# Performance work log

Measured on AMD Instinct MI355X. Metric: run time of the kernel, lower is better.

## Reference

```python
import jax, jax.numpy as jnp
import numpy as np

N_NODES = 100000
N_EDGES = 600000
N_ETYPES = 3
N_LAYERS = 3  # n_layers + 1 conv layers
D = 128
EPS = 1e-5


def setup_inputs() -> dict:
    key = jax.random.key(0)
    ks = jax.random.split(key, 8)
    scale = 1.0 / np.sqrt(D)
    x = jax.random.normal(ks[0], (N_NODES, D), dtype=jnp.float32)
    src = jax.random.randint(ks[1], (N_ETYPES, N_EDGES), 0, N_NODES, dtype=jnp.int32)
    dst = jax.random.randint(ks[2], (N_ETYPES, N_EDGES), 0, N_NODES, dtype=jnp.int32)
    W_self = jax.random.normal(ks[3], (N_LAYERS, N_ETYPES, D, D), dtype=jnp.float32) * scale
    W_neigh = jax.random.normal(ks[4], (N_LAYERS, N_ETYPES, D, D), dtype=jnp.float32) * scale
    b = jax.random.normal(ks[5], (N_LAYERS, N_ETYPES, D), dtype=jnp.float32) * 0.01
    gamma = jnp.ones((N_LAYERS, D), dtype=jnp.float32)
    beta = jnp.zeros((N_LAYERS, D), dtype=jnp.float32)
    return {"x": x, "src": src, "dst": dst, "W_self": W_self, "W_neigh": W_neigh,
            "b": b, "gamma": gamma, "beta": beta}


def reference(x, src, dst, W_self, W_neigh, b, gamma, beta):
    N = x.shape[0]
    L, K = W_self.shape[0], W_self.shape[1]
    # in-degree per etype (DGL mean aggregator: zero-degree -> 0 neighbor feat)
    degs = [jnp.clip(jax.ops.segment_sum(jnp.ones((dst.shape[1],), x.dtype), dst[k],
                                         num_segments=N), 1.0, None)
            for k in range(K)]
    h = x
    for l in range(L):
        acc = jnp.zeros((N, W_self.shape[-1]), x.dtype)
        for k in range(K):
            # gather src feats, mean-aggregate onto dst: [N, D]
            neigh = jax.ops.segment_sum(h[src[k]], dst[k], num_segments=N) / degs[k][:, None]
            o = h @ W_self[l, k] + neigh @ W_neigh[l, k] + b[l, k]
            if l < L - 1:  # activation inside SAGEConv, last layer has none
                o = jax.nn.relu(o)
            acc = acc + o  # HeteroGraphConv aggregate='sum'
        # BatchNorm1d, training mode (biased batch variance)
        mu = acc.mean(axis=0)
        var = ((acc - mu) ** 2).mean(axis=0)
        h = gamma[l] * (acc - mu) / jnp.sqrt(var + EPS) + beta[l]
    return h
```

## Files before the change

kernel.cpp:

```cpp
#include <hip/hip_runtime.h>

#define NN 100000
#define NNP 100096
#define NE 600000
#define KE 3
#define NL 3
#define D  128
#define EPS 1e-5f
#define NB 391
#define NBKT 196
#define EPB 4096
#define NEB 147
#define NSL 16

typedef __attribute__((ext_vector_type(8))) short short8;
typedef __attribute__((ext_vector_type(4))) float floatx4;

__device__ __forceinline__ void atomic_add_f32(float* p, float v) { unsafeAtomicAdd(p, v); }

__device__ __forceinline__ float bf2f(unsigned int u16) {
    unsigned int v = u16 << 16;
    return __builtin_bit_cast(float, v);
}
__device__ __forceinline__ unsigned int f2bf(float f) {
    unsigned int u = __builtin_bit_cast(unsigned int, f);
    u += 0x7FFFu + ((u >> 16) & 1u);
    return u >> 16;
}
__device__ __forceinline__ unsigned int pack2(float a, float b) {
    return f2bf(a) | (f2bf(b) << 16);
}

__global__ void convert_x_kernel(const float* __restrict__ x, ushort* __restrict__ hbf) {
    size_t i = (size_t)blockIdx.x * blockDim.x + threadIdx.x;
    if (i >= (size_t)NN * D / 4) return;
    float4 v = *(const float4*)(x + i * 4);
    uint2 o;
    o.x = pack2(v.x, v.y);
    o.y = pack2(v.z, v.w);
    *(uint2*)(hbf + i * 4) = o;
}

__global__ void wprep_kernel(const float* __restrict__ Ws, const float* __restrict__ Wn,
                             ushort* __restrict__ Bt) {
    int idx = blockIdx.x * blockDim.x + threadIdx.x;
    if (idx >= NL * KE * 128 * 256) return;
    int lk  = idx >> 15;
    int rem = idx & 32767;
    int n   = rem >> 8;
    int kk  = rem & 255;
    float v = (kk < 128) ? Ws[(size_t)lk * 16384 + kk * 128 + n]
                         : Wn[(size_t)lk * 16384 + (kk - 128) * 128 + n];
    Bt[idx] = (ushort)f2bf(v);
}

__global__ void bucket_count_kernel(const int* __restrict__ dst,
                                    int* __restrict__ bucketTotal, int* __restrict__ blockBase) {
    const int blk = blockIdx.x;
    const int k = blk / NEB, cb = blk - k * NEB;
    __shared__ int hist[NBKT];
    for (int i = threadIdx.x; i < NBKT; i += 256) hist[i] = 0;
    __syncthreads();
    const int e0 = cb * EPB, e1 = min(e0 + EPB, NE);
    for (int e = e0 + threadIdx.x; e < e1; e += 256)
        atomicAdd(&hist[dst[(size_t)k * NE + e] >> 9], 1);
    __syncthreads();
    for (int i = threadIdx.x; i < NBKT; i += 256) {
        int c = hist[i];
        int base = c ? atomicAdd(&bucketTotal[k * NBKT + i], c) : 0;
        blockBase[(size_t)blk * NBKT + i] = base;
    }
}

__global__ void bucket_scan_kernel(const int* __restrict__ bucketTotal,
                                   int* __restrict__ bucketStart) {
    __shared__ int sd[1024];
    const int t = threadIdx.x;
    int v = (t < KE * NBKT) ? bucketTotal[t] : 0;
    sd[t] = v;
    __syncthreads();
    for (int off = 1; off < 1024; off <<= 1) {
        int u = (t >= off) ? sd[t - off] : 0;
        __syncthreads();
        sd[t] += u;
        __syncthreads();
    }
    if (t < KE * NBKT) bucketStart[t] = sd[t] - v;
}

__global__ void bucket_scatter_kernel(const int* __restrict__ src, const int* __restrict__ dst,
                                      const int* __restrict__ bucketStart,
                                      const int* __restrict__ blockBase,
                                      uint2* __restrict__ ebuf) {
    const int blk = blockIdx.x;
    const int k = blk / NEB, cb = blk - k * NEB;
    __shared__ int hist[NBKT], binoff[NBKT], cur[NBKT];
    __shared__ int sc[256];
    __shared__ uint2 stage[EPB];
    const int t = threadIdx.x;
    for (int i = t; i < NBKT; i += 256) hist[i] = 0;
    __syncthreads();
    const int e0 = cb * EPB, e1 = min(e0 + EPB, NE);
    for (int e = e0 + t; e < e1; e += 256)
        atomicAdd(&hist[dst[(size_t)k * NE + e] >> 9], 1);
    __syncthreads();
    int hv = (t < NBKT) ? hist[t] : 0;
    sc[t] = hv;
    __syncthreads();
    for (int off = 1; off < 256; off <<= 1) {
        int u = (t >= off) ? sc[t - off] : 0;
        __syncthreads();
        sc[t] += u;
        __syncthreads();
    }
    if (t < NBKT) { binoff[t] = sc[t] - hv; cur[t] = sc[t] - hv; }
    __syncthreads();
    for (int e = e0 + t; e < e1; e += 256) {
        int d = dst[(size_t)k * NE + e], s = src[(size_t)k * NE + e];
        int b = d >> 9;
        int p = atomicAdd(&cur[b], 1);
        stage[p] = make_uint2((unsigned)s, (unsigned)d);
    }
    __syncthreads();
    const int n = e1 - e0;
    for (int i = t; i < n; i += 256) {
        uint2 ed = stage[i];
        int b = (int)(ed.y >> 9);
        int pos = bucketStart[k * NBKT + b] + blockBase[(size_t)blk * NBKT + b] + (i - binoff[b]);
        ebuf[pos] = ed;
    }
}

__global__ void bucket_deg_kernel(const uint2* __restrict__ ebuf,
                                  const int* __restrict__ bucketStart, int* __restrict__ degi) {
    const int blk = blockIdx.x;
    const int k = blk / NBKT, b = blk - k * NBKT;
    __shared__ int cnt[512];
    for (int i = threadIdx.x; i < 512; i += 256) cnt[i] = 0;
    __syncthreads();
    const int s0 = bucketStart[blk];
    const int s1 = (blk + 1 < KE * NBKT) ? bucketStart[blk + 1] : KE * NE;
    for (int e = s0 + threadIdx.x; e < s1; e += 256)
        atomicAdd(&cnt[ebuf[e].y & 511], 1);
    __syncthreads();
    const int n0 = b << 9;
    for (int i = threadIdx.x; i < 512; i += 256) {
        int node = n0 + i;
        if (node < NN) degi[(size_t)k * NN + node] = cnt[i];
    }
}

__global__ void scan_a_kernel(const int* __restrict__ degi, int* __restrict__ bsum) {
    const int b = blockIdx.x;
    const int k = b / NB, lb = b - k * NB;
    const int t = threadIdx.x;
    const int i = lb * 256 + t;
    int deg = (i < NN) ? degi[(size_t)k * NN + i] : 0;
    __shared__ int sd[256];
    sd[t] = deg;
    __syncthreads();
    for (int off = 128; off > 0; off >>= 1) {
        if (t < off) sd[t] += sd[t + off];
        __syncthreads();
    }
    if (t == 0) bsum[b] = sd[0];
}

__global__ void scan_b_kernel(int* __restrict__ bsum) {
    const int k = blockIdx.x;
    const int t = threadIdx.x;
    int v = (t < NB) ? bsum[k * NB + t] : 0;
    __shared__ int sd[512];
    sd[t] = v;
    __syncthreads();
    for (int off = 1; off < 512; off <<= 1) {
        int u = (t >= off) ? sd[t - off] : 0;
        __syncthreads();
        sd[t] += u;
        __syncthreads();
    }
    if (t < NB) bsum[k * NB + t] = sd[t] - v;
}

__global__ void scan_c_kernel(const int* __restrict__ degi, const int* __restrict__ bsum,
                              int* __restrict__ rowptr, float* __restrict__ invdeg) {
    const int b = blockIdx.x;
    const int k = b / NB, lb = b - k * NB;
    const int t = threadIdx.x;
    const int i = lb * 256 + t;
    int deg = (i < NN) ? degi[(size_t)k * NN + i] : 0;
    __shared__ int sd[256];
    sd[t] = deg;
    __syncthreads();
    for (int off = 1; off < 256; off <<= 1) {
        int u = (t >= off) ? sd[t - off] : 0;
        __syncthreads();
        sd[t] += u;
        __syncthreads();
    }
    int val = bsum[b] + sd[t] - deg;
    if (i < NN) {
        rowptr[(size_t)k * (NN + 1) + i] = val;
        invdeg[(size_t)k * NN + i] = 1.0f / (float)max(deg, 1);
    }
    if (i == NN) rowptr[(size_t)k * (NN + 1) + NN] = NE;
}

__global__ void bucket_fill_kernel(const uint2* __restrict__ ebuf,
                                   const int* __restrict__ bucketStart,
                                   const int* __restrict__ rowptr, int* __restrict__ csr) {
    const int blk = blockIdx.x;
    const int k = blk / NBKT, b = blk - k * NBKT;
    __shared__ int cur[512];
    const int n0 = b << 9;
    for (int i = threadIdx.x; i < 512; i += 256) {
        int node = n0 + i;
        cur[i] = (node < NN) ? rowptr[(size_t)k * (NN + 1) + node] : 0;
    }
    __syncthreads();
    const int s0 = bucketStart[blk];
    const int s1 = (blk + 1 < KE * NBKT) ? bucketStart[blk + 1] : KE * NE;
    for (int e = s0 + threadIdx.x; e < s1; e += 256) {
        uint2 ed = ebuf[e];
        int p = atomicAdd(&cur[ed.y & 511], 1);
        csr[(size_t)k * NE + p] = (int)ed.x;
    }
}

__global__ void gather3_kernel(const ushort* __restrict__ hbf, const int* __restrict__ csr,
                               const int* __restrict__ rowptr, const float* __restrict__ invdeg,
                               ushort* __restrict__ neigh) {
    int g = blockIdx.x * 16 + (threadIdx.x >> 4);
    if (g >= KE * NN) return;
    int k = g / NN, node = g - k * NN;
    const int q = (threadIdx.x & 15) * 8;
    const int* rp = rowptr + (size_t)k * (NN + 1) + node;
    const int* cs = csr + (size_t)k * NE;
    int beg = rp[0], end = rp[1];
    float f0=0,f1=0,f2=0,f3=0,f4=0,f5=0,f6=0,f7=0;
    int j = beg;
    for (; j + 4 <= end; j += 4) {
        int s0 = cs[j], s1 = cs[j + 1], s2 = cs[j + 2], s3 = cs[j + 3];
        uint4 a = *(const uint4*)(hbf + (size_t)s0 * D + q);
        uint4 b = *(const uint4*)(hbf + (size_t)s1 * D + q);
        uint4 c = *(const uint4*)(hbf + (size_t)s2 * D + q);
        uint4 d = *(const uint4*)(hbf + (size_t)s3 * D + q);
        f0 += bf2f(a.x & 0xffff) + bf2f(b.x & 0xffff) + bf2f(c.x & 0xffff) + bf2f(d.x & 0xffff);
        f1 += bf2f(a.x >> 16)    + bf2f(b.x >> 16)    + bf2f(c.x >> 16)    + bf2f(d.x >> 16);
        f2 += bf2f(a.y & 0xffff) + bf2f(b.y & 0xffff) + bf2f(c.y & 0xffff) + bf2f(d.y & 0xffff);
        f3 += bf2f(a.y >> 16)    + bf2f(b.y >> 16)    + bf2f(c.y >> 16)    + bf2f(d.y >> 16);
        f4 += bf2f(a.z & 0xffff) + bf2f(b.z & 0xffff) + bf2f(c.z & 0xffff) + bf2f(d.z & 0xffff);
        f5 += bf2f(a.z >> 16)    + bf2f(b.z >> 16)    + bf2f(c.z >> 16)    + bf2f(d.z >> 16);
        f6 += bf2f(a.w & 0xffff) + bf2f(b.w & 0xffff) + bf2f(c.w & 0xffff) + bf2f(d.w & 0xffff);
        f7 += bf2f(a.w >> 16)    + bf2f(b.w >> 16)    + bf2f(c.w >> 16)    + bf2f(d.w >> 16);
    }
    for (; j < end; ++j) {
        int s0 = cs[j];
        uint4 a = *(const uint4*)(hbf + (size_t)s0 * D + q);
        f0 += bf2f(a.x & 0xffff); f1 += bf2f(a.x >> 16);
        f2 += bf2f(a.y & 0xffff); f3 += bf2f(a.y >> 16);
        f4 += bf2f(a.z & 0xffff); f5 += bf2f(a.z >> 16);
        f6 += bf2f(a.w & 0xffff); f7 += bf2f(a.w >> 16);
    }
    float sc = invdeg[g];
    uint4 o;
    o.x = pack2(f0 * sc, f1 * sc);
    o.y = pack2(f2 * sc, f3 * sc);
    o.z = pack2(f4 * sc, f5 * sc);
    o.w = pack2(f6 * sc, f7 * sc);
    *(uint4*)(neigh + (size_t)k * NNP * D + (size_t)node * D + q) = o;
}

__global__ __launch_bounds__(256, 2)
void layer_gemm_kernel(const ushort* __restrict__ hbf, const ushort* __restrict__ neigh,
                       const ushort* __restrict__ Bt,
                       const float* __restrict__ bias,
                       ushort* __restrict__ accb, int relu,
                       float* __restrict__ colsum, float* __restrict__ colsq) {
    __shared__ __align__(16) ushort shbuf[2][128][72];
#define As shbuf[0]
#define Bs shbuf[1]
    const int tid  = threadIdx.x;
    const int wave = tid >> 6, lane = tid & 63;
    const int wm = wave & 1, wn = wave >> 1;
    const int lrow = lane & 15, quad = lane >> 4;
    const int m0 = blockIdx.x * 128;
    const int ldrow = tid >> 3;
    const int ldcol = (tid & 7) * 8;

    floatx4 tot[4][4];
    #pragma unroll
    for (int a = 0; a < 4; ++a)
        #pragma unroll
        for (int b = 0; b < 4; ++b)
            tot[a][b] = (floatx4){0.f, 0.f, 0.f, 0.f};

    for (int k = 0; k < KE; ++k) {
        floatx4 o[4][4];
        #pragma unroll
        for (int a = 0; a < 4; ++a)
            #pragma unroll
            for (int b = 0; b < 4; ++b)
                o[a][b] = (floatx4){0.f, 0.f, 0.f, 0.f};

        for (int part = 0; part < 2; ++part) {
            const ushort* Asrc = part ? (neigh + (size_t)k * NNP * D) : hbf;
            #pragma unroll
            for (int kc = 0; kc < 2; ++kc) {
                __syncthreads();
                const int kbase = kc * 64;
                #pragma unroll
                for (int p = 0; p < 4; ++p) {
                    int r = p * 32 + ldrow;
                    uint4 v = *(const uint4*)(Asrc + (size_t)(m0 + r) * D + kbase + ldcol);
                    *(uint4*)(&As[r][ldcol]) = v;
                }
                const ushort* Bsrc = Bt + (size_t)k * 128 * 256 + part * 128 + kbase;
                #pragma unroll
                for (int p = 0; p < 4; ++p) {
                    int n = p * 32 + ldrow;
                    uint4 v = *(const uint4*)(Bsrc + (size_t)n * 256 + ldcol);
                    *(uint4*)(&Bs[n][ldcol]) = v;
                }
                __syncthreads();
                #pragma unroll
                for (int ks = 0; ks < 2; ++ks) {
                    short8 af[4], bfr[4];
                    const int koff = ks * 32 + quad * 8;
                    #pragma unroll
                    for (int im = 0; im < 4; ++im)
                        af[im] = *(const short8*)(&As[wm * 64 + im * 16 + lrow][koff]);
                    #pragma unroll
                    for (int in = 0; in < 4; ++in)
                        bfr[in] = *(const short8*)(&Bs[wn * 64 + in * 16 + lrow][koff]);
                    #pragma unroll
                    for (int im = 0; im < 4; ++im)
                        #pragma unroll
                        for (int in = 0; in < 4; ++in)
                            o[im][in] = __builtin_amdgcn_mfma_f32_16x16x32_bf16(
                                af[im], bfr[in], o[im][in], 0, 0, 0);
                }
            }
        }
        const float* bk = bias + k * D;
        float bv[4];
        #pragma unroll
        for (int in = 0; in < 4; ++in) bv[in] = bk[wn * 64 + in * 16 + lrow];
        #pragma unroll
        for (int im = 0; im < 4; ++im)
            #pragma unroll
            for (int in = 0; in < 4; ++in)
                #pragma unroll
                for (int r = 0; r < 4; ++r) {
                    float v = o[im][in][r] + bv[in];
                    if (relu) v = fmaxf(v, 0.f);
                    tot[im][in][r] += v;
                }
    }

    float ls[4] = {0.f, 0.f, 0.f, 0.f}, lq[4] = {0.f, 0.f, 0.f, 0.f};
    #pragma unroll
    for (int im = 0; im < 4; ++im)
        #pragma unroll
        for (int r = 0; r < 4; ++r) {
            int row = m0 + wm * 64 + im * 16 + quad * 4 + r;
            bool ok = row < NN;
            #pragma unroll
            for (int in = 0; in < 4; ++in) {
                float v = ok ? tot[im][in][r] : 0.f;
                ls[in] += v;
                lq[in] += v * v;
            }
        }
    __syncthreads();
    float* redS = (float*)&shbuf[0][0][0];
    float* redQ = ((float*)&shbuf[0][0][0]) + 1024;
    #pragma unroll
    for (int in = 0; in < 4; ++in) {
        int col = wn * 64 + in * 16 + lrow;
        int slot = col * 8 + wm * 4 + quad;
        redS[slot] = ls[in];
        redQ[slot] = lq[in];
    }
    __syncthreads();
    if (tid < 128) {
        float s = 0.f, q = 0.f;
        #pragma unroll
        for (int i = 0; i < 8; ++i) { s += redS[tid * 8 + i]; q += redQ[tid * 8 + i]; }
        int slice = blockIdx.x & (NSL - 1);
        atomic_add_f32(&colsum[slice * D + tid], s);
        atomic_add_f32(&colsq[slice * D + tid], q);
    }
    __syncthreads();

    ushort* Cs = &shbuf[0][0][0];
    #pragma unroll
    for (int im = 0; im < 4; ++im)
        #pragma unroll
        for (int r = 0; r < 4; ++r) {
            int rl = wm * 64 + im * 16 + quad * 4 + r;
            #pragma unroll
            for (int in = 0; in < 4; ++in)
                Cs[rl * 128 + wn * 64 + in * 16 + lrow] = (ushort)f2bf(tot[im][in][r]);
        }
    __syncthreads();
    #pragma unroll
    for (int jj = 0; jj < 8; ++jj) {
        int c8 = tid + jj * 256;
        int rl = c8 >> 4;
        int cc = (c8 & 15) * 8;
        int row = m0 + rl;
        if (row < NN)
            *(uint4*)(accb + (size_t)row * D + cc) = *(const uint4*)(Cs + rl * 128 + cc);
    }
#undef As
#undef Bs
}

__global__ void finalize_kernel(const float* __restrict__ colsum, const float* __restrict__ colsq,
                                const float* __restrict__ gamma, const float* __restrict__ beta,
                                float* __restrict__ ss) {
    int c = threadIdx.x;
    float s = 0.f, q = 0.f;
    #pragma unroll
    for (int i = 0; i < NSL; ++i) { s += colsum[i * D + c]; q += colsq[i * D + c]; }
    float mu  = s * (1.0f / NN);
    float var = q * (1.0f / NN) - mu * mu;
    float sc  = gamma[c] * rsqrtf(var + EPS);
    ss[c]     = sc;
    ss[D + c] = beta[c] - mu * sc;
}

__global__ void bn_kernel(const ushort* __restrict__ accb, const float* __restrict__ ss,
                          ushort* __restrict__ hbf, float* __restrict__ out, int last) {
    size_t i = (size_t)blockIdx.x * blockDim.x + threadIdx.x;
    if (i >= (size_t)NN * D / 4) return;
    int c4 = (int)(i & 31) << 2;
    uint2 a = *(const uint2*)(accb + i * 4);
    float4 v = {bf2f(a.x & 0xffff), bf2f(a.x >> 16), bf2f(a.y & 0xffff), bf2f(a.y >> 16)};
    float4 sc = *(const float4*)(ss + c4);
    float4 sh = *(const float4*)(ss + D + c4);
    float4 o;
    o.x = v.x * sc.x + sh.x;
    o.y = v.y * sc.y + sh.y;
    o.z = v.z * sc.z + sh.z;
    o.w = v.w * sc.w + sh.w;
    if (last) {
        *(float4*)(out + i * 4) = o;
    } else {
        uint2 p;
        p.x = pack2(o.x, o.y);
        p.y = pack2(o.z, o.w);
        *(uint2*)(hbf + i * 4) = p;
    }
}

extern "C" void kernel_launch(void* const* d_in, const int* in_sizes, int n_in,
                              void* d_out, int out_size, void* d_ws, size_t ws_size,
                              hipStream_t stream) {
    const float* x       = (const float*)d_in[0];
    const int*   src     = (const int*)d_in[1];
    const int*   dst     = (const int*)d_in[2];
    const float* W_self  = (const float*)d_in[3];
    const float* W_neigh = (const float*)d_in[4];
    const float* bvec    = (const float*)d_in[5];
    const float* gamma   = (const float*)d_in[6];
    const float* beta    = (const float*)d_in[7];
    float* out = (float*)d_out;

    ushort* accb   = (ushort*)d_ws;
    float*  invdeg = (float*)(accb + (size_t)NNP * D);
    float*  colsum = invdeg + (size_t)KE * NN;
    float*  colsq  = colsum + NSL * D;
    float*  ss     = colsq + NSL * D;
    ushort* hbf    = (ushort*)(ss + 2 * D);
    ushort* neigh  = hbf + (size_t)NNP * D;
    ushort* Btw    = neigh + (size_t)KE * NNP * D;
    int*    degi   = (int*)(Btw + (size_t)NL * KE * 128 * 256);
    int*    rowptr = degi + (size_t)KE * NN;
    int*    csr    = rowptr + (size_t)KE * (NN + 1);
    int*    bsum   = csr + (size_t)KE * NE;
    int*    bucketTotal = bsum + (size_t)KE * NB;
    int*    bucketStart = bucketTotal + KE * NBKT;
    int*    blockBase   = bucketStart + KE * NBKT;
    uint2*  ebuf   = (uint2*)accb;

    convert_x_kernel<<<(int)(((size_t)NN * D / 4 + 255) / 256), 256, 0, stream>>>(x, hbf);
    wprep_kernel<<<(NL * KE * 128 * 256 + 255) / 256, 256, 0, stream>>>(W_self, W_neigh, Btw);

    hipMemsetAsync(bucketTotal, 0, sizeof(int) * KE * NBKT, stream);
    bucket_count_kernel<<<KE * NEB, 256, 0, stream>>>(dst, bucketTotal, blockBase);
    bucket_scan_kernel<<<1, 1024, 0, stream>>>(bucketTotal, bucketStart);
    bucket_scatter_kernel<<<KE * NEB, 256, 0, stream>>>(src, dst, bucketStart, blockBase, ebuf);
    bucket_deg_kernel<<<KE * NBKT, 256, 0, stream>>>(ebuf, bucketStart, degi);
    scan_a_kernel<<<KE * NB, 256, 0, stream>>>(degi, bsum);
    scan_b_kernel<<<KE, 512, 0, stream>>>(bsum);
    scan_c_kernel<<<KE * NB, 256, 0, stream>>>(degi, bsum, rowptr, invdeg);
    bucket_fill_kernel<<<KE * NBKT, 256, 0, stream>>>(ebuf, bucketStart, rowptr, csr);

    for (int l = 0; l < NL; ++l) {
        int relu = (l < NL - 1) ? 1 : 0;
        gather3_kernel<<<(KE * NN + 15) / 16, 256, 0, stream>>>(hbf, csr, rowptr, invdeg, neigh);
        hipMemsetAsync(colsum, 0, sizeof(float) * 2 * NSL * D, stream);
        layer_gemm_kernel<<<NNP / 128, 256, 0, stream>>>(
            hbf, neigh,
            Btw + (size_t)l * KE * 128 * 256,
            bvec + (size_t)l * KE * D,
            accb, relu, colsum, colsq);
        finalize_kernel<<<1, 128, 0, stream>>>(colsum, colsq, gamma + (size_t)l * D,
                                               beta + (size_t)l * D, ss);
        bn_kernel<<<(int)(((size_t)NN * D / 4 + 255) / 256), 256, 0, stream>>>(
            accb, ss, hbf, out, (l == NL - 1) ? 1 : 0);
    }
}
```

Baseline: 599.4 us.

## Fold BatchNorm affine into next layer weights and gather; use direct-to-LDS loads

Drops the per-layer BatchNorm pass over the node features. The BN scale is folded into the next layer's self-weight matrix and the BN shift into its bias, and the gather applies the affine to neighbor means on the fly, skipping nodes with no in-edges. The GEMM now reads the raw pre-BN bf16 accumulator directly and stages tiles with global_load_lds into an XOR-swizzled, unpadded LDS layout. The per-layer memset is moved into finalize. The fold adds a small serial kernel per layer and applies the BN scale to the bf16 weights, which changes rounding.

```diff
diff --git a/kernel.cpp b/kernel.cpp
--- a/kernel.cpp
+++ b/kernel.cpp
@@ -31,6 +31,12 @@
     return f2bf(a) | (f2bf(b) << 16);
 }
 
+__device__ __forceinline__ void gload16(const void* g, void* l) {
+    __builtin_amdgcn_global_load_lds(
+        (const __attribute__((address_space(1))) void*)g,
+        (__attribute__((address_space(3))) void*)l, 16, 0, 0);
+}
+
 __global__ void convert_x_kernel(const float* __restrict__ x, ushort* __restrict__ hbf) {
     size_t i = (size_t)blockIdx.x * blockDim.x + threadIdx.x;
     if (i >= (size_t)NN * D / 4) return;
@@ -54,6 +60,23 @@
     Bt[idx] = (ushort)f2bf(v);
 }
 
+__global__ void fold_kernel(const float* __restrict__ Wsl, const float* __restrict__ bsrc,
+                            const float* __restrict__ ssl, ushort* __restrict__ Btl,
+                            float* __restrict__ biasW) {
+    const int k = blockIdx.x;
+    const int n = threadIdx.x;
+    const float* W = Wsl + (size_t)k * D * D;
+    ushort* B = Btl + (size_t)k * 32768;
+    float acc = 0.f;
+    #pragma unroll 4
+    for (int kk = 0; kk < D; ++kk) {
+        float w = W[kk * D + n];
+        acc += ssl[D + kk] * w;
+        B[n * 256 + kk] = (ushort)f2bf(ssl[kk] * w);
+    }
+    biasW[k * D + n] = bsrc[k * D + n] + acc;
+}
+
 __global__ void bucket_count_kernel(const int* __restrict__ dst,
                                     int* __restrict__ bucketTotal, int* __restrict__ blockBase) {
     const int blk = blockIdx.x;
@@ -227,9 +250,10 @@
     }
 }
 
-__global__ void gather3_kernel(const ushort* __restrict__ hbf, const int* __restrict__ csr,
+__global__ void gather3_kernel(const ushort* __restrict__ hsrc, const int* __restrict__ csr,
                                const int* __restrict__ rowptr, const float* __restrict__ invdeg,
-                               ushort* __restrict__ neigh) {
+                               ushort* __restrict__ neigh, const float* __restrict__ ssl,
+                               int affine) {
     int g = blockIdx.x * 16 + (threadIdx.x >> 4);
     if (g >= KE * NN) return;
     int k = g / NN, node = g - k * NN;
@@ -241,10 +265,10 @@
     int j = beg;
     for (; j + 4 <= end; j += 4) {
         int s0 = cs[j], s1 = cs[j + 1], s2 = cs[j + 2], s3 = cs[j + 3];
-        uint4 a = *(const uint4*)(hbf + (size_t)s0 * D + q);
-        uint4 b = *(const uint4*)(hbf + (size_t)s1 * D + q);
-        uint4 c = *(const uint4*)(hbf + (size_t)s2 * D + q);
-        uint4 d = *(const uint4*)(hbf + (size_t)s3 * D + q);
+        uint4 a = *(const uint4*)(hsrc + (size_t)s0 * D + q);
+        uint4 b = *(const uint4*)(hsrc + (size_t)s1 * D + q);
+        uint4 c = *(const uint4*)(hsrc + (size_t)s2 * D + q);
+        uint4 d = *(const uint4*)(hsrc + (size_t)s3 * D + q);
         f0 += bf2f(a.x & 0xffff) + bf2f(b.x & 0xffff) + bf2f(c.x & 0xffff) + bf2f(d.x & 0xffff);
         f1 += bf2f(a.x >> 16)    + bf2f(b.x >> 16)    + bf2f(c.x >> 16)    + bf2f(d.x >> 16);
         f2 += bf2f(a.y & 0xffff) + bf2f(b.y & 0xffff) + bf2f(c.y & 0xffff) + bf2f(d.y & 0xffff);
@@ -256,37 +280,52 @@
     }
     for (; j < end; ++j) {
         int s0 = cs[j];
-        uint4 a = *(const uint4*)(hbf + (size_t)s0 * D + q);
+        uint4 a = *(const uint4*)(hsrc + (size_t)s0 * D + q);
         f0 += bf2f(a.x & 0xffff); f1 += bf2f(a.x >> 16);
         f2 += bf2f(a.y & 0xffff); f3 += bf2f(a.y >> 16);
         f4 += bf2f(a.z & 0xffff); f5 += bf2f(a.z >> 16);
         f6 += bf2f(a.w & 0xffff); f7 += bf2f(a.w >> 16);
     }
-    float sc = invdeg[g];
+    float iv = invdeg[g];
+    float r0 = f0 * iv, r1 = f1 * iv, r2 = f2 * iv, r3 = f3 * iv;
+    float r4 = f4 * iv, r5 = f5 * iv, r6 = f6 * iv, r7 = f7 * iv;
+    if (affine) {
+        float4 c0 = *(const float4*)(ssl + q);
+        float4 c1 = *(const float4*)(ssl + q + 4);
+        float4 h0 = *(const float4*)(ssl + D + q);
+        float4 h1 = *(const float4*)(ssl + D + q + 4);
+        float m = (end > beg) ? 1.0f : 0.0f;
+        r0 = r0 * c0.x + m * h0.x;  r1 = r1 * c0.y + m * h0.y;
+        r2 = r2 * c0.z + m * h0.z;  r3 = r3 * c0.w + m * h0.w;
+        r4 = r4 * c1.x + m * h1.x;  r5 = r5 * c1.y + m * h1.y;
+        r6 = r6 * c1.z + m * h1.z;  r7 = r7 * c1.w + m * h1.w;
+    }
     uint4 o;
-    o.x = pack2(f0 * sc, f1 * sc);
-    o.y = pack2(f2 * sc, f3 * sc);
-    o.z = pack2(f4 * sc, f5 * sc);
-    o.w = pack2(f6 * sc, f7 * sc);
+    o.x = pack2(r0, r1);
+    o.y = pack2(r2, r3);
+    o.z = pack2(r4, r5);
+    o.w = pack2(r6, r7);
     *(uint4*)(neigh + (size_t)k * NNP * D + (size_t)node * D + q) = o;
 }
 
 __global__ __launch_bounds__(256, 2)
-void layer_gemm_kernel(const ushort* __restrict__ hbf, const ushort* __restrict__ neigh,
+void layer_gemm_kernel(const ushort* __restrict__ hself, const ushort* __restrict__ neigh,
                        const ushort* __restrict__ Bt,
                        const float* __restrict__ bias,
                        ushort* __restrict__ accb, int relu,
                        float* __restrict__ colsum, float* __restrict__ colsq) {
-    __shared__ __align__(16) ushort shbuf[2][128][72];
-#define As shbuf[0]
-#define Bs shbuf[1]
+    __shared__ __align__(16) ushort shbuf[2][128][64];
     const int tid  = threadIdx.x;
     const int wave = tid >> 6, lane = tid & 63;
     const int wm = wave & 1, wn = wave >> 1;
     const int lrow = lane & 15, quad = lane >> 4;
     const int m0 = blockIdx.x * 128;
-    const int ldrow = tid >> 3;
-    const int ldcol = (tid & 7) * 8;
+    const int srow  = lane >> 3;
+    const int scolb = (((lane & 7) ^ srow) << 4);
+    char* AsL = (char*)&shbuf[0][0][0] + wave * 4096;
+    char* BsL = (char*)&shbuf[1][0][0] + wave * 4096;
+    const char* AsR = (const char*)&shbuf[0][0][0];
+    const char* BsR = (const char*)&shbuf[1][0][0];
 
     floatx4 tot[4][4];
     #pragma unroll
@@ -302,37 +341,40 @@
             #pragma unroll
             for (int b = 0; b < 4; ++b)
                 o[a][b] = (floatx4){0.f, 0.f, 0.f, 0.f};
+        const char* Btk = (const char*)Bt + (size_t)k * 65536;
 
         for (int part = 0; part < 2; ++part) {
-            const ushort* Asrc = part ? (neigh + (size_t)k * NNP * D) : hbf;
+            const ushort* Asrc = part ? (neigh + (size_t)k * NNP * D) : hself;
             #pragma unroll
             for (int kc = 0; kc < 2; ++kc) {
                 __syncthreads();
-                const int kbase = kc * 64;
                 #pragma unroll
-                for (int p = 0; p < 4; ++p) {
-                    int r = p * 32 + ldrow;
-                    uint4 v = *(const uint4*)(Asrc + (size_t)(m0 + r) * D + kbase + ldcol);
-                    *(uint4*)(&As[r][ldcol]) = v;
+                for (int i = 0; i < 4; ++i) {
+                    int r = wave * 32 + i * 8 + srow;
+                    gload16((const char*)Asrc + (size_t)(m0 + r) * 256 + kc * 128 + scolb,
+                            AsL + i * 1024);
                 }
-                const ushort* Bsrc = Bt + (size_t)k * 128 * 256 + part * 128 + kbase;
                 #pragma unroll
-                for (int p = 0; p < 4; ++p) {
-                    int n = p * 32 + ldrow;
-                    uint4 v = *(const uint4*)(Bsrc + (size_t)n * 256 + ldcol);
-                    *(uint4*)(&Bs[n][ldcol]) = v;
+                for (int i = 0; i < 4; ++i) {
+                    int n = wave * 32 + i * 8 + srow;
+                    gload16(Btk + (size_t)n * 512 + part * 256 + kc * 128 + scolb,
+                            BsL + i * 1024);
                 }
                 __syncthreads();
                 #pragma unroll
                 for (int ks = 0; ks < 2; ++ks) {
                     short8 af[4], bfr[4];
-                    const int koff = ks * 32 + quad * 8;
+                    const int cb = ks * 64 + quad * 16;
                     #pragma unroll
-                    for (int im = 0; im < 4; ++im)
-                        af[im] = *(const short8*)(&As[wm * 64 + im * 16 + lrow][koff]);
+                    for (int im = 0; im < 4; ++im) {
+                        int ra = wm * 64 + im * 16 + lrow;
+                        af[im] = *(const short8*)(AsR + ra * 128 + (cb ^ ((ra & 7) << 4)));
+                    }
                     #pragma unroll
-                    for (int in = 0; in < 4; ++in)
-                        bfr[in] = *(const short8*)(&Bs[wn * 64 + in * 16 + lrow][koff]);
+                    for (int in = 0; in < 4; ++in) {
+                        int rb = wn * 64 + in * 16 + lrow;
+                        bfr[in] = *(const short8*)(BsR + rb * 128 + (cb ^ ((rb & 7) << 4)));
+                    }
                     #pragma unroll
                     for (int im = 0; im < 4; ++im)
                         #pragma unroll
@@ -413,13 +455,11 @@
         if (row < NN)
             *(uint4*)(accb + (size_t)row * D + cc) = *(const uint4*)(Cs + rl * 128 + cc);
     }
-#undef As
-#undef Bs
-}
-
-__global__ void finalize_kernel(const float* __restrict__ colsum, const float* __restrict__ colsq,
+}
+
+__global__ void finalize_kernel(float* __restrict__ colsum, float* __restrict__ colsq,
                                 const float* __restrict__ gamma, const float* __restrict__ beta,
-                                float* __restrict__ ss) {
+                                float* __restrict__ ssl) {
     int c = threadIdx.x;
     float s = 0.f, q = 0.f;
     #pragma unroll
@@ -427,32 +467,27 @@
     float mu  = s * (1.0f / NN);
     float var = q * (1.0f / NN) - mu * mu;
     float sc  = gamma[c] * rsqrtf(var + EPS);
-    ss[c]     = sc;
-    ss[D + c] = beta[c] - mu * sc;
-}
-
-__global__ void bn_kernel(const ushort* __restrict__ accb, const float* __restrict__ ss,
-                          ushort* __restrict__ hbf, float* __restrict__ out, int last) {
+    ssl[c]     = sc;
+    ssl[D + c] = beta[c] - mu * sc;
+    #pragma unroll
+    for (int i = 0; i < NSL; ++i) { colsum[i * D + c] = 0.f; colsq[i * D + c] = 0.f; }
+}
+
+__global__ void bn_kernel(const ushort* __restrict__ accb, const float* __restrict__ ssl,
+                          float* __restrict__ out) {
     size_t i = (size_t)blockIdx.x * blockDim.x + threadIdx.x;
     if (i >= (size_t)NN * D / 4) return;
     int c4 = (int)(i & 31) << 2;
     uint2 a = *(const uint2*)(accb + i * 4);
     float4 v = {bf2f(a.x & 0xffff), bf2f(a.x >> 16), bf2f(a.y & 0xffff), bf2f(a.y >> 16)};
-    float4 sc = *(const float4*)(ss + c4);
-    float4 sh = *(const float4*)(ss + D + c4);
+    float4 sc = *(const float4*)(ssl + c4);
+    float4 sh = *(const float4*)(ssl + D + c4);
     float4 o;
     o.x = v.x * sc.x + sh.x;
     o.y = v.y * sc.y + sh.y;
     o.z = v.z * sc.z + sh.z;
     o.w = v.w * sc.w + sh.w;
-    if (last) {
-        *(float4*)(out + i * 4) = o;
-    } else {
-        uint2 p;
-        p.x = pack2(o.x, o.y);
-        p.y = pack2(o.z, o.w);
-        *(uint2*)(hbf + i * 4) = p;
-    }
+    *(float4*)(out + i * 4) = o;
 }
 
 extern "C" void kernel_launch(void* const* d_in, const int* in_sizes, int n_in,
@@ -473,7 +508,8 @@
     float*  colsum = invdeg + (size_t)KE * NN;
     float*  colsq  = colsum + NSL * D;
     float*  ss     = colsq + NSL * D;
-    ushort* hbf    = (ushort*)(ss + 2 * D);
+    float*  biasW  = ss + NL * 2 * D;
+    ushort* hbf    = (ushort*)(biasW + KE * D);
     ushort* neigh  = hbf + (size_t)NNP * D;
     ushort* Btw    = neigh + (size_t)KE * NNP * D;
     int*    degi   = (int*)(Btw + (size_t)NL * KE * 128 * 256);
@@ -487,6 +523,7 @@
 
     convert_x_kernel<<<(int)(((size_t)NN * D / 4 + 255) / 256), 256, 0, stream>>>(x, hbf);
     wprep_kernel<<<(NL * KE * 128 * 256 + 255) / 256, 256, 0, stream>>>(W_self, W_neigh, Btw);
+    hipMemsetAsync(colsum, 0, sizeof(float) * 2 * NSL * D, stream);
 
     hipMemsetAsync(bucketTotal, 0, sizeof(int) * KE * NBKT, stream);
     bucket_count_kernel<<<KE * NEB, 256, 0, stream>>>(dst, bucketTotal, blockBase);
@@ -500,16 +537,25 @@
 
     for (int l = 0; l < NL; ++l) {
         int relu = (l < NL - 1) ? 1 : 0;
-        gather3_kernel<<<(KE * NN + 15) / 16, 256, 0, stream>>>(hbf, csr, rowptr, invdeg, neigh);
-        hipMemsetAsync(colsum, 0, sizeof(float) * 2 * NSL * D, stream);
+        const ushort* hsrc = (l == 0) ? hbf : accb;
+        const float*  ssl  = ss + (size_t)(l ? l - 1 : 0) * 2 * D;
+        gather3_kernel<<<(KE * NN + 15) / 16, 256, 0, stream>>>(
+            hsrc, csr, rowptr, invdeg, neigh, ssl, l > 0);
         layer_gemm_kernel<<<NNP / 128, 256, 0, stream>>>(
-            hbf, neigh,
+            hsrc, neigh,
             Btw + (size_t)l * KE * 128 * 256,
-            bvec + (size_t)l * KE * D,
+            (l == 0) ? bvec : biasW,
             accb, relu, colsum, colsq);
         finalize_kernel<<<1, 128, 0, stream>>>(colsum, colsq, gamma + (size_t)l * D,
-                                               beta + (size_t)l * D, ss);
-        bn_kernel<<<(int)(((size_t)NN * D / 4 + 255) / 256), 256, 0, stream>>>(
-            accb, ss, hbf, out, (l == NL - 1) ? 1 : 0);
-    }
-}
+                                               beta + (size_t)l * D, ss + (size_t)l * 2 * D);
+        if (l + 1 < NL)
+            fold_kernel<<<KE, 128, 0, stream>>>(
+                W_self + (size_t)(l + 1) * KE * D * D,
+                bvec + (size_t)(l + 1) * KE * D,
+                ss + (size_t)l * 2 * D,
+                Btw + (size_t)(l + 1) * KE * 128 * 256,
+                biasW);
+    }
+    bn_kernel<<<(int)(((size_t)NN * D / 4 + 255) / 256), 256, 0, stream>>>(
+        accb, ss + (size_t)(NL - 1) * 2 * D, out);
+}
```

After: 572.4 us. 1.05x faster.
